# Kernel tuning notes

Hardware: AMD Instinct MI355X
Metric: run time of the kernel (lower is better)

Reference implementation:

```python
import jax, jax.numpy as jnp
import numpy as np

B, N, K, C = 8, 8192, 16, 64
POS_HID, MULT = 64, 4
BN_EPS = 1e-3  # keras BatchNormalization default


def _bn(x, gamma, beta):
    # inference-mode BN with init moving stats (mean=0, var=1)
    return gamma * x * (1.0 / np.sqrt(1.0 + BN_EPS)) + beta


def setup_inputs() -> dict:
    key = jax.random.key(0)
    ks = jax.random.split(key, 16)
    d = {
        "key": jax.random.normal(ks[0], (B, N, C), jnp.float32),
        "query": jax.random.normal(ks[1], (B, N, C), jnp.float32),
        "value": jax.random.normal(ks[2], (B, N, C), jnp.float32),
        "pos": jax.random.normal(ks[3], (B, N, 3), jnp.float32),
        "idx": jax.random.randint(ks[4], (B, N, K), 0, N, jnp.int32),
        # pos_conv1: 1x1 conv 3 -> POS_HID (glorot), + BN params
        "W1": jax.random.normal(ks[5], (3, POS_HID), jnp.float32) * np.sqrt(2.0 / (3 + POS_HID)),
        "b1": jnp.zeros((POS_HID,), jnp.float32),
        "g1": jnp.ones((POS_HID,), jnp.float32) + 0.1 * jax.random.normal(ks[6], (POS_HID,), jnp.float32),
        "bt1": 0.1 * jax.random.normal(ks[7], (POS_HID,), jnp.float32),
        # pos_conv2: POS_HID -> C, no activation
        "W2": jax.random.normal(ks[8], (POS_HID, C), jnp.float32) * np.sqrt(2.0 / (POS_HID + C)),
        "b2": jnp.zeros((C,), jnp.float32),
        # attn_mlp1: C -> MULT*C, BN + relu
        "W3": jax.random.normal(ks[9], (C, MULT * C), jnp.float32) * np.sqrt(2.0 / (C + MULT * C)),
        "b3": jnp.zeros((MULT * C,), jnp.float32),
        "g3": jnp.ones((MULT * C,), jnp.float32) + 0.1 * jax.random.normal(ks[10], (MULT * C,), jnp.float32),
        "bt3": 0.1 * jax.random.normal(ks[11], (MULT * C,), jnp.float32),
        # attn_mlp2: MULT*C -> C, no activation
        "W4": jax.random.normal(ks[12], (MULT * C, C), jnp.float32) * np.sqrt(2.0 / (MULT * C + C)),
        "b4": jnp.zeros((C,), jnp.float32),
    }
    return d


def reference(key, query, value, pos, idx, W1, b1, g1, bt1, W2, b2, W3, b3, g3, bt3, W4, b4):
    # per-batch KNN gather: key [B,N,C], idx [B,N,K] -> [B,N,K,C]
    gather = jax.vmap(lambda t, i: t[i])
    k_nb = gather(key, idx)                         # [B,N,K,C]
    qk_rel = query[:, :, None, :] - k_nb            # [B,N,K,C]
    pos_rel = pos[:, :, None, :] - gather(pos, idx)  # [B,N,K,3]

    # positional embedding MLP (1x1 convs)
    h = jax.nn.relu(_bn(pos_rel @ W1 + b1, g1, bt1))  # [B,N,K,POS_HID]
    pos_em = h @ W2 + b2                              # [B,N,K,C]

    # attention MLP (subtraction-based vector attention)
    a = jax.nn.relu(_bn((qk_rel + pos_em) @ W3 + b3, g3, bt3))  # [B,N,K,4C]
    a = (a @ W4 + b4) / jnp.sqrt(jnp.asarray(C, jnp.float32))   # [B,N,K,C]
    # tf.nn.softmax default axis=-1 -> softmax over CHANNEL axis (faithful to source)
    a = jax.nn.softmax(a, axis=-1)

    v = value[:, :, None, :] + pos_em               # [B,N,K,C]
    # einsum 'b c i j, b c i j -> b c j' on channels-last: sum over neighbor axis K
    agg = jnp.sum(a * v, axis=2)                    # [B,N,C]
    return agg
```

## Files before the change

### kernel.cpp

```cpp
#include <hip/hip_runtime.h>
#include <hip/hip_bf16.h>

typedef __bf16 bf16x8 __attribute__((ext_vector_type(8)));
typedef float  f32x4  __attribute__((ext_vector_type(4)));

#define MFMA16(A,B,C) __builtin_amdgcn_mfma_f32_16x16x32_bf16((A),(B),(C),0,0,0)

constexpr int NB = 8, NN = 8192, KK = 16;
constexpr size_t WS_NEEDED = 75776;


__global__ void prep_kernel(const float* __restrict__ W1, const float* __restrict__ b1,
                            const float* __restrict__ g1, const float* __restrict__ bt1,
                            const float* __restrict__ W2, const float* __restrict__ W3,
                            const float* __restrict__ b3, const float* __restrict__ g3,
                            const float* __restrict__ bt3, const float* __restrict__ W4,
                            unsigned char* __restrict__ ws)
{
    __bf16* w3f = (__bf16*)(ws);
    __bf16* w4f = (__bf16*)(ws + 32768);
    __bf16* w2f = (__bf16*)(ws + 65536);
    float*  W1f = (float*)(ws + 73728);
    float*  c1f = (float*)(ws + 74496);
    float*  c3f = (float*)(ws + 74752);

    const float inv = 1.0f / sqrtf(1.0f + 1e-3f);
    int t = blockIdx.x * 256 + threadIdx.x;

    if (t < 16384) {
        int i = t & 7, lane = (t >> 3) & 63, r = t >> 9;
        int ks = r & 1, nb = r >> 1;
        int k = ks * 32 + (lane >> 4) * 8 + i;
        int n = nb * 16 + (lane & 15);
        w3f[t] = (__bf16)(W3[k * 256 + n] * (g3[n] * inv));
    } else if (t < 32768) {
        int u = t - 16384;
        int i = u & 7, lane = (u >> 3) & 63, r = u >> 9;
        int kb = r & 7, nb = r >> 3;
        int k = kb * 32 + (lane >> 4) * 8 + i;
        int n = nb * 16 + (lane & 15);
        w4f[u] = (__bf16)(W4[k * 64 + n] * 0.125f);
    } else if (t < 36864) {
        int u = t - 32768;
        int i = u & 7, lane = (u >> 3) & 63, r = u >> 9;
        int ks = r & 1, nb = r >> 1;
        int k = ks * 32 + (lane >> 4) * 8 + i;
        int n = nb * 16 + (lane & 15);
        w2f[u] = (__bf16)(W2[k * 64 + n]);
    } else if (t < 37056) {
        int u = t - 36864;
        int c = u & 63;
        W1f[u] = W1[u] * (g1[c] * inv);
    } else if (t < 37120) {
        int c = t - 37056;
        c1f[c] = b1[c] * (g1[c] * inv) + bt1[c];
    } else if (t < 37376) {
        int n = t - 37120;
        c3f[n] = b3[n] * (g3[n] * inv) + bt3[n];
    }
}

__global__ __launch_bounds__(256, 2) void fused_kernel(
    const float* __restrict__ key, const float* __restrict__ query,
    const float* __restrict__ value, const float* __restrict__ pos,
    const int* __restrict__ idx, const float* __restrict__ b2,
    const float* __restrict__ b4, const unsigned char* __restrict__ ws,
    float* __restrict__ out)
{
    const __bf16* w3f = (const __bf16*)(ws);
    const __bf16* w4f = (const __bf16*)(ws + 32768);
    const __bf16* w2f = (const __bf16*)(ws + 65536);
    const float*  W1f = (const float*)(ws + 73728);
    const float*  c1f = (const float*)(ws + 74496);
    const float*  c3f = (const float*)(ws + 74752);

    __shared__ __attribute__((aligned(16))) __bf16 sX [4][2048];
    __shared__ __attribute__((aligned(16))) __bf16 sA1[4][2048];
    __shared__ __attribute__((aligned(16))) float  sPR[4][32][4];
    __shared__ int sJ[4][32];

    const int wv   = threadIdx.x >> 6;
    const int lane = threadIdx.x & 63;
    const int lg   = lane >> 4;
    const int ln   = lane & 15;

    const int ptbase = blockIdx.x * 8 + wv * 2;
    const int b  = ptbase >> 13;
    const int n0 = ptbase & 8191;

    __bf16* X  = sX[wv];
    __bf16* A1 = sA1[wv];

    if (lane < 32) {
        int p = lane >> 4, k = lane & 15;
        int n = n0 + p;
        int j = idx[(b * NN + n) * KK + k];
        sJ[wv][lane] = j;
        int pb = (b * NN + n) * 3, jb = (b * NN + j) * 3;
        sPR[wv][lane][0] = pos[pb + 0] - pos[jb + 0];
        sPR[wv][lane][1] = pos[pb + 1] - pos[jb + 1];
        sPR[wv][lane][2] = pos[pb + 2] - pos[jb + 2];
        sPR[wv][lane][3] = 0.f;
    }
    {
        float w0 = W1f[lane], w1 = W1f[64 + lane], w2c = W1f[128 + lane], cc1 = c1f[lane];
        for (int r = 0; r < 32; ++r) {
            float4 pr = *(const float4*)&sPR[wv][r][0];
            float hv = fmaf(pr.x, w0, fmaf(pr.y, w1, fmaf(pr.z, w2c, cc1)));
            hv = fmaxf(hv, 0.f);
            X[(r * 64 + lane) ^ ((r & 7) << 3)] = (__bf16)hv;
        }
    }

    bf16x8 hf[2][2];
    #pragma unroll
    for (int rb = 0; rb < 2; ++rb)
        #pragma unroll
        for (int ks = 0; ks < 2; ++ks) {
            int row = rb * 16 + ln;
            hf[rb][ks] = *(const bf16x8*)&X[(row * 64 + ks * 32 + lg * 8) ^ ((row & 7) << 3)];
        }
    f32x4 pacc[2][4];
    #pragma unroll
    for (int rb = 0; rb < 2; ++rb)
        #pragma unroll
        for (int cb = 0; cb < 4; ++cb) pacc[rb][cb] = f32x4{0.f, 0.f, 0.f, 0.f};
    #pragma unroll
    for (int cb = 0; cb < 4; ++cb)
        #pragma unroll
        for (int ks = 0; ks < 2; ++ks) {
            bf16x8 wf = *(const bf16x8*)(w2f + (size_t)((cb * 2 + ks) * 64 + lane) * 8);
            pacc[0][cb] = MFMA16(hf[0][ks], wf, pacc[0][cb]);
            pacc[1][cb] = MFMA16(hf[1][ks], wf, pacc[1][cb]);
        }

    float posem[2][4][4];
    #pragma unroll
    for (int rb = 0; rb < 2; ++rb) {
        const int nrow = n0 + rb;
        float qv[4];
        #pragma unroll
        for (int cb = 0; cb < 4; ++cb) {
            qv[cb] = query[(b * NN + nrow) * 64 + cb * 16 + ln];
            float c2v = b2[cb * 16 + ln];
            #pragma unroll
            for (int jj = 0; jj < 4; ++jj)
                posem[rb][cb][jj] = pacc[rb][cb][jj] + c2v;
        }
        #pragma unroll
        for (int jj = 0; jj < 4; ++jj) {
            int row = rb * 16 + lg * 4 + jj;
            int jb = (b * NN + sJ[wv][row]) * 64;
            #pragma unroll
            for (int cb = 0; cb < 4; ++cb) {
                float x = qv[cb] - key[jb + cb * 16 + ln] + posem[rb][cb][jj];
                X[(row * 64 + cb * 16 + ln) ^ ((row & 7) << 3)] = (__bf16)x;
            }
        }
    }

    bf16x8 xf[2][2];
    #pragma unroll
    for (int rb = 0; rb < 2; ++rb)
        #pragma unroll
        for (int ks = 0; ks < 2; ++ks) {
            int row = rb * 16 + ln;
            xf[rb][ks] = *(const bf16x8*)&X[(row * 64 + ks * 32 + lg * 8) ^ ((row & 7) << 3)];
        }
    f32x4 acc2[2][4];
    #pragma unroll
    for (int rb = 0; rb < 2; ++rb)
        #pragma unroll
        for (int nb = 0; nb < 4; ++nb) acc2[rb][nb] = f32x4{0.f, 0.f, 0.f, 0.f};

    for (int cc = 0; cc < 4; ++cc) {
        f32x4 g1a[2][4];
        #pragma unroll
        for (int rb = 0; rb < 2; ++rb)
            #pragma unroll
            for (int cb = 0; cb < 4; ++cb) g1a[rb][cb] = f32x4{0.f, 0.f, 0.f, 0.f};
        #pragma unroll
        for (int cb = 0; cb < 4; ++cb) {
            int nb = cc * 4 + cb;
            #pragma unroll
            for (int ks = 0; ks < 2; ++ks) {
                bf16x8 wf = *(const bf16x8*)(w3f + (size_t)((nb * 2 + ks) * 64 + lane) * 8);
                g1a[0][cb] = MFMA16(xf[0][ks], wf, g1a[0][cb]);
                g1a[1][cb] = MFMA16(xf[1][ks], wf, g1a[1][cb]);
            }
        }
        #pragma unroll
        for (int cb = 0; cb < 4; ++cb) {
            float c3v = c3f[(cc * 4 + cb) * 16 + ln];
            #pragma unroll
            for (int rb = 0; rb < 2; ++rb)
                #pragma unroll
                for (int jj = 0; jj < 4; ++jj) {
                    int row = rb * 16 + lg * 4 + jj;
                    float v = fmaxf(g1a[rb][cb][jj] + c3v, 0.f);
                    A1[(row * 64 + cb * 16 + ln) ^ ((row & 7) << 3)] = (__bf16)v;
                }
        }
        #pragma unroll
        for (int kb2 = 0; kb2 < 2; ++kb2) {
            bf16x8 a1f[2];
            #pragma unroll
            for (int rb = 0; rb < 2; ++rb) {
                int row = rb * 16 + ln;
                a1f[rb] = *(const bf16x8*)&A1[(row * 64 + kb2 * 32 + lg * 8) ^ ((row & 7) << 3)];
            }
            #pragma unroll
            for (int nb = 0; nb < 4; ++nb) {
                bf16x8 wf = *(const bf16x8*)(w4f + (size_t)((nb * 8 + cc * 2 + kb2) * 64 + lane) * 8);
                acc2[0][nb] = MFMA16(a1f[0], wf, acc2[0][nb]);
                acc2[1][nb] = MFMA16(a1f[1], wf, acc2[1][nb]);
            }
        }
    }

    #pragma unroll
    for (int rb = 0; rb < 2; ++rb) {
        const int nrow = n0 + rb;
        float val[4][4];
        #pragma unroll
        for (int nb = 0; nb < 4; ++nb) {
            float b4v = b4[nb * 16 + ln] * 0.125f;
            #pragma unroll
            for (int jj = 0; jj < 4; ++jj) val[nb][jj] = acc2[rb][nb][jj] + b4v;
        }
        float vv[4];
        #pragma unroll
        for (int nb = 0; nb < 4; ++nb) vv[nb] = value[(b * NN + nrow) * 64 + nb * 16 + ln];

        float res[4] = {0.f, 0.f, 0.f, 0.f};
        #pragma unroll
        for (int jj = 0; jj < 4; ++jj) {
            float m = fmaxf(fmaxf(val[0][jj], val[1][jj]), fmaxf(val[2][jj], val[3][jj]));
            #pragma unroll
            for (int d = 1; d < 16; d <<= 1) m = fmaxf(m, __shfl_xor(m, d, 64));
            float e0 = __expf(val[0][jj] - m), e1 = __expf(val[1][jj] - m);
            float e2 = __expf(val[2][jj] - m), e3 = __expf(val[3][jj] - m);
            float s = e0 + e1 + e2 + e3;
            #pragma unroll
            for (int d = 1; d < 16; d <<= 1) s += __shfl_xor(s, d, 64);
            float inv = 1.0f / s;
            res[0] = fmaf(e0 * inv, vv[0] + posem[rb][0][jj], res[0]);
            res[1] = fmaf(e1 * inv, vv[1] + posem[rb][1][jj], res[1]);
            res[2] = fmaf(e2 * inv, vv[2] + posem[rb][2][jj], res[2]);
            res[3] = fmaf(e3 * inv, vv[3] + posem[rb][3][jj], res[3]);
        }
        #pragma unroll
        for (int nb = 0; nb < 4; ++nb) {
            res[nb] += __shfl_xor(res[nb], 16, 64);
            res[nb] += __shfl_xor(res[nb], 32, 64);
        }
        float o = (lg == 0) ? res[0] : (lg == 1) ? res[1] : (lg == 2) ? res[2] : res[3];
        out[(b * NN + nrow) * 64 + lane] = o;
    }
}

extern "C" void kernel_launch(void* const* d_in, const int* in_sizes, int n_in,
                              void* d_out, int out_size, void* d_ws, size_t ws_size,
                              hipStream_t stream) {
    const float* key   = (const float*)d_in[0];
    const float* query = (const float*)d_in[1];
    const float* value = (const float*)d_in[2];
    const float* pos   = (const float*)d_in[3];
    const int*   idx   = (const int*)d_in[4];
    const float* W1    = (const float*)d_in[5];
    const float* b1    = (const float*)d_in[6];
    const float* g1    = (const float*)d_in[7];
    const float* bt1   = (const float*)d_in[8];
    const float* W2    = (const float*)d_in[9];
    const float* b2    = (const float*)d_in[10];
    const float* W3    = (const float*)d_in[11];
    const float* b3    = (const float*)d_in[12];
    const float* g3    = (const float*)d_in[13];
    const float* bt3   = (const float*)d_in[14];
    const float* W4    = (const float*)d_in[15];
    const float* b4    = (const float*)d_in[16];
    unsigned char* ws  = (unsigned char*)d_ws;
    float* out = (float*)d_out;

    if (ws_size < WS_NEEDED) return;

    hipLaunchKernelGGL(prep_kernel, dim3(146), dim3(256), 0, stream,
                       W1, b1, g1, bt1, W2, W3, b3, g3, bt3, W4, ws);
    hipLaunchKernelGGL(fused_kernel, dim3(8192), dim3(256), 0, stream,
                       key, query, value, pos, idx, b2, b4, ws, out);
}
```

Before: 305.1 us.

## Permute channel layout for vector LDS stores, MFMA pos-conv1, drop softmax max

Permutes the K dimension of W2/W3/W4 in the prep kernel so each lane can write its four channel values as one bf16x4 store into a padded (stride 72) LDS tile, replacing the XOR-swizzled scalar stores. The first positional 1x1 conv (3->64 with folded bias) now runs as an MFMA with a homogeneous-coordinate column instead of a scalar loop over 32 rows. The softmax max-subtraction and its shuffle reduction are removed, which risks overflow if logits grow large.

After: 262.0 us. -14.1%, faster.

```diff
diff --git a/kernel.cpp b/kernel.cpp
--- a/kernel.cpp
+++ b/kernel.cpp
@@ -2,12 +2,14 @@
 #include <hip/hip_bf16.h>
 
 typedef __bf16 bf16x8 __attribute__((ext_vector_type(8)));
+typedef __bf16 bf16x4 __attribute__((ext_vector_type(4)));
 typedef float  f32x4  __attribute__((ext_vector_type(4)));
 
 #define MFMA16(A,B,C) __builtin_amdgcn_mfma_f32_16x16x32_bf16((A),(B),(C),0,0,0)
 
 constexpr int NB = 8, NN = 8192, KK = 16;
-constexpr size_t WS_NEEDED = 75776;
+constexpr int XS = 72;
+constexpr size_t WS_NEEDED = 78848;
 
 
 __global__ void prep_kernel(const float* __restrict__ W1, const float* __restrict__ b1,
@@ -20,9 +22,8 @@
     __bf16* w3f = (__bf16*)(ws);
     __bf16* w4f = (__bf16*)(ws + 32768);
     __bf16* w2f = (__bf16*)(ws + 65536);
-    float*  W1f = (float*)(ws + 73728);
-    float*  c1f = (float*)(ws + 74496);
-    float*  c3f = (float*)(ws + 74752);
+    __bf16* w1f = (__bf16*)(ws + 73728);
+    float*  c3f = (float*)(ws + 77824);
 
     const float inv = 1.0f / sqrtf(1.0f + 1e-3f);
     int t = blockIdx.x * 256 + threadIdx.x;
@@ -30,32 +31,37 @@
     if (t < 16384) {
         int i = t & 7, lane = (t >> 3) & 63, r = t >> 9;
         int ks = r & 1, nb = r >> 1;
-        int k = ks * 32 + (lane >> 4) * 8 + i;
+        int p = ks * 32 + (lane >> 4) * 8 + i;
+        int c = (p & 3) * 16 + (p >> 2);
         int n = nb * 16 + (lane & 15);
-        w3f[t] = (__bf16)(W3[k * 256 + n] * (g3[n] * inv));
+        w3f[t] = (__bf16)(W3[c * 256 + n] * (g3[n] * inv));
     } else if (t < 32768) {
         int u = t - 16384;
         int i = u & 7, lane = (u >> 3) & 63, r = u >> 9;
         int kb = r & 7, nb = r >> 3;
-        int k = kb * 32 + (lane >> 4) * 8 + i;
+        int q = (kb & 1) * 32 + (lane >> 4) * 8 + i;
+        int c = (kb >> 1) * 64 + (q & 3) * 16 + (q >> 2);
         int n = nb * 16 + (lane & 15);
-        w4f[u] = (__bf16)(W4[k * 64 + n] * 0.125f);
+        w4f[u] = (__bf16)(W4[c * 64 + n] * 0.125f);
     } else if (t < 36864) {
         int u = t - 32768;
         int i = u & 7, lane = (u >> 3) & 63, r = u >> 9;
         int ks = r & 1, nb = r >> 1;
-        int k = ks * 32 + (lane >> 4) * 8 + i;
+        int p = ks * 32 + (lane >> 4) * 8 + i;
+        int c = (p & 3) * 16 + (p >> 2);
         int n = nb * 16 + (lane & 15);
-        w2f[u] = (__bf16)(W2[k * 64 + n]);
-    } else if (t < 37056) {
+        w2f[u] = (__bf16)(W2[c * 64 + n]);
+    } else if (t < 38912) {
         int u = t - 36864;
-        int c = u & 63;
-        W1f[u] = W1[u] * (g1[c] * inv);
-    } else if (t < 37120) {
-        int c = t - 37056;
-        c1f[c] = b1[c] * (g1[c] * inv) + bt1[c];
-    } else if (t < 37376) {
-        int n = t - 37120;
+        int i = u & 7, lane = (u >> 3) & 63, nb = u >> 9;
+        int kk = (lane >> 4) * 8 + i;
+        int n = nb * 16 + (lane & 15);
+        float v = 0.f;
+        if (kk < 3)       v = W1[kk * 64 + n] * (g1[n] * inv);
+        else if (kk == 3) v = b1[n] * (g1[n] * inv) + bt1[n];
+        w1f[u] = (__bf16)v;
+    } else if (t < 39168) {
+        int n = t - 38912;
         c3f[n] = b3[n] * (g3[n] * inv) + bt3[n];
     }
 }
@@ -70,12 +76,13 @@
     const __bf16* w3f = (const __bf16*)(ws);
     const __bf16* w4f = (const __bf16*)(ws + 32768);
     const __bf16* w2f = (const __bf16*)(ws + 65536);
-    const float*  W1f = (const float*)(ws + 73728);
-    const float*  c1f = (const float*)(ws + 74496);
-    const float*  c3f = (const float*)(ws + 74752);
-
-    __shared__ __attribute__((aligned(16))) __bf16 sX [4][2048];
-    __shared__ __attribute__((aligned(16))) __bf16 sA1[4][2048];
+    const __bf16* w1f = (const __bf16*)(ws + 73728);
+    const float*  c3f = (const float*)(ws + 77824);
+
+    const f32x4 ZERO4 = {0.f, 0.f, 0.f, 0.f};
+
+    __shared__ __attribute__((aligned(16))) __bf16 sX [4][32 * XS];
+    __shared__ __attribute__((aligned(16))) __bf16 sA1[4][32 * XS];
     __shared__ __attribute__((aligned(16))) float  sPR[4][32][4];
     __shared__ int sJ[4][32];
 
@@ -102,29 +109,48 @@
         sPR[wv][lane][2] = pos[pb + 2] - pos[jb + 2];
         sPR[wv][lane][3] = 0.f;
     }
-    {
-        float w0 = W1f[lane], w1 = W1f[64 + lane], w2c = W1f[128 + lane], cc1 = c1f[lane];
-        for (int r = 0; r < 32; ++r) {
-            float4 pr = *(const float4*)&sPR[wv][r][0];
-            float hv = fmaf(pr.x, w0, fmaf(pr.y, w1, fmaf(pr.z, w2c, cc1)));
-            hv = fmaxf(hv, 0.f);
-            X[(r * 64 + lane) ^ ((r & 7) << 3)] = (__bf16)hv;
-        }
-    }
+    bf16x8 af[2];
+    #pragma unroll
+    for (int rb = 0; rb < 2; ++rb) {
+        bf16x8 a;
+        #pragma unroll
+        for (int i = 0; i < 8; ++i) a[i] = (__bf16)0.0f;
+        if (lg == 0) {
+            const float4 pr = *(const float4*)&sPR[wv][rb * 16 + ln][0];
+            a[0] = (__bf16)pr.x; a[1] = (__bf16)pr.y; a[2] = (__bf16)pr.z;
+            a[3] = (__bf16)1.0f;
+        }
+        af[rb] = a;
+    }
+    f32x4 pa[2][4];
+    #pragma unroll
+    for (int nb = 0; nb < 4; ++nb) {
+        bf16x8 wf = *(const bf16x8*)(w1f + (size_t)(nb * 64 + lane) * 8);
+        pa[0][nb] = MFMA16(af[0], wf, ZERO4);
+        pa[1][nb] = MFMA16(af[1], wf, ZERO4);
+    }
+    #pragma unroll
+    for (int rb = 0; rb < 2; ++rb)
+        #pragma unroll
+        for (int jj = 0; jj < 4; ++jj) {
+            int row = rb * 16 + lg * 4 + jj;
+            bf16x4 hv;
+            #pragma unroll
+            for (int nb = 0; nb < 4; ++nb) hv[nb] = (__bf16)fmaxf(pa[rb][nb][jj], 0.f);
+            *(bf16x4*)&X[row * XS + ln * 4] = hv;
+        }
 
     bf16x8 hf[2][2];
     #pragma unroll
     for (int rb = 0; rb < 2; ++rb)
         #pragma unroll
-        for (int ks = 0; ks < 2; ++ks) {
-            int row = rb * 16 + ln;
-            hf[rb][ks] = *(const bf16x8*)&X[(row * 64 + ks * 32 + lg * 8) ^ ((row & 7) << 3)];
-        }
+        for (int ks = 0; ks < 2; ++ks)
+            hf[rb][ks] = *(const bf16x8*)&X[(rb * 16 + ln) * XS + ks * 32 + lg * 8];
     f32x4 pacc[2][4];
     #pragma unroll
     for (int rb = 0; rb < 2; ++rb)
         #pragma unroll
-        for (int cb = 0; cb < 4; ++cb) pacc[rb][cb] = f32x4{0.f, 0.f, 0.f, 0.f};
+        for (int cb = 0; cb < 4; ++cb) pacc[rb][cb] = ZERO4;
     #pragma unroll
     for (int cb = 0; cb < 4; ++cb)
         #pragma unroll
@@ -151,11 +177,11 @@
         for (int jj = 0; jj < 4; ++jj) {
             int row = rb * 16 + lg * 4 + jj;
             int jb = (b * NN + sJ[wv][row]) * 64;
-            #pragma unroll
-            for (int cb = 0; cb < 4; ++cb) {
-                float x = qv[cb] - key[jb + cb * 16 + ln] + posem[rb][cb][jj];
-                X[(row * 64 + cb * 16 + ln) ^ ((row & 7) << 3)] = (__bf16)x;
-            }
+            bf16x4 xv;
+            #pragma unroll
+            for (int cb = 0; cb < 4; ++cb)
+                xv[cb] = (__bf16)(qv[cb] - key[jb + cb * 16 + ln] + posem[rb][cb][jj]);
+            *(bf16x4*)&X[row * XS + ln * 4] = xv;
         }
     }
 
@@ -163,22 +189,20 @@
     #pragma unroll
     for (int rb = 0; rb < 2; ++rb)
         #pragma unroll
-        for (int ks = 0; ks < 2; ++ks) {
-            int row = rb * 16 + ln;
-            xf[rb][ks] = *(const bf16x8*)&X[(row * 64 + ks * 32 + lg * 8) ^ ((row & 7) << 3)];
-        }
+        for (int ks = 0; ks < 2; ++ks)
+            xf[rb][ks] = *(const bf16x8*)&X[(rb * 16 + ln) * XS + ks * 32 + lg * 8];
     f32x4 acc2[2][4];
     #pragma unroll
     for (int rb = 0; rb < 2; ++rb)
         #pragma unroll
-        for (int nb = 0; nb < 4; ++nb) acc2[rb][nb] = f32x4{0.f, 0.f, 0.f, 0.f};
+        for (int nb = 0; nb < 4; ++nb) acc2[rb][nb] = ZERO4;
 
     for (int cc = 0; cc < 4; ++cc) {
         f32x4 g1a[2][4];
         #pragma unroll
         for (int rb = 0; rb < 2; ++rb)
             #pragma unroll
-            for (int cb = 0; cb < 4; ++cb) g1a[rb][cb] = f32x4{0.f, 0.f, 0.f, 0.f};
+            for (int cb = 0; cb < 4; ++cb) g1a[rb][cb] = ZERO4;
         #pragma unroll
         for (int cb = 0; cb < 4; ++cb) {
             int nb = cc * 4 + cb;
@@ -189,26 +213,26 @@
                 g1a[1][cb] = MFMA16(xf[1][ks], wf, g1a[1][cb]);
             }
         }
-        #pragma unroll
-        for (int cb = 0; cb < 4; ++cb) {
-            float c3v = c3f[(cc * 4 + cb) * 16 + ln];
-            #pragma unroll
-            for (int rb = 0; rb < 2; ++rb)
+        float c3v[4];
+        #pragma unroll
+        for (int cb = 0; cb < 4; ++cb) c3v[cb] = c3f[(cc * 4 + cb) * 16 + ln];
+        #pragma unroll
+        for (int rb = 0; rb < 2; ++rb)
+            #pragma unroll
+            for (int jj = 0; jj < 4; ++jj) {
+                int row = rb * 16 + lg * 4 + jj;
+                bf16x4 av;
                 #pragma unroll
-                for (int jj = 0; jj < 4; ++jj) {
-                    int row = rb * 16 + lg * 4 + jj;
-                    float v = fmaxf(g1a[rb][cb][jj] + c3v, 0.f);
-                    A1[(row * 64 + cb * 16 + ln) ^ ((row & 7) << 3)] = (__bf16)v;
-                }
-        }
+                for (int cb = 0; cb < 4; ++cb)
+                    av[cb] = (__bf16)fmaxf(g1a[rb][cb][jj] + c3v[cb], 0.f);
+                *(bf16x4*)&A1[row * XS + ln * 4] = av;
+            }
         #pragma unroll
         for (int kb2 = 0; kb2 < 2; ++kb2) {
             bf16x8 a1f[2];
             #pragma unroll
-            for (int rb = 0; rb < 2; ++rb) {
-                int row = rb * 16 + ln;
-                a1f[rb] = *(const bf16x8*)&A1[(row * 64 + kb2 * 32 + lg * 8) ^ ((row & 7) << 3)];
-            }
+            for (int rb = 0; rb < 2; ++rb)
+                a1f[rb] = *(const bf16x8*)&A1[(rb * 16 + ln) * XS + kb2 * 32 + lg * 8];
             #pragma unroll
             for (int nb = 0; nb < 4; ++nb) {
                 bf16x8 wf = *(const bf16x8*)(w4f + (size_t)((nb * 8 + cc * 2 + kb2) * 64 + lane) * 8);
@@ -218,16 +242,12 @@
         }
     }
 
+    float b4v[4];
+    #pragma unroll
+    for (int nb = 0; nb < 4; ++nb) b4v[nb] = b4[nb * 16 + ln] * 0.125f;
     #pragma unroll
     for (int rb = 0; rb < 2; ++rb) {
         const int nrow = n0 + rb;
-        float val[4][4];
-        #pragma unroll
-        for (int nb = 0; nb < 4; ++nb) {
-            float b4v = b4[nb * 16 + ln] * 0.125f;
-            #pragma unroll
-            for (int jj = 0; jj < 4; ++jj) val[nb][jj] = acc2[rb][nb][jj] + b4v;
-        }
         float vv[4];
         #pragma unroll
         for (int nb = 0; nb < 4; ++nb) vv[nb] = value[(b * NN + nrow) * 64 + nb * 16 + ln];
@@ -235,12 +255,11 @@
         float res[4] = {0.f, 0.f, 0.f, 0.f};
         #pragma unroll
         for (int jj = 0; jj < 4; ++jj) {
-            float m = fmaxf(fmaxf(val[0][jj], val[1][jj]), fmaxf(val[2][jj], val[3][jj]));
-            #pragma unroll
-            for (int d = 1; d < 16; d <<= 1) m = fmaxf(m, __shfl_xor(m, d, 64));
-            float e0 = __expf(val[0][jj] - m), e1 = __expf(val[1][jj] - m);
-            float e2 = __expf(val[2][jj] - m), e3 = __expf(val[3][jj] - m);
-            float s = e0 + e1 + e2 + e3;
+            float e0 = __expf(acc2[rb][0][jj] + b4v[0]);
+            float e1 = __expf(acc2[rb][1][jj] + b4v[1]);
+            float e2 = __expf(acc2[rb][2][jj] + b4v[2]);
+            float e3 = __expf(acc2[rb][3][jj] + b4v[3]);
+            float s = (e0 + e1) + (e2 + e3);
             #pragma unroll
             for (int d = 1; d < 16; d <<= 1) s += __shfl_xor(s, d, 64);
             float inv = 1.0f / s;
@@ -284,7 +303,7 @@
 
     if (ws_size < WS_NEEDED) return;
 
-    hipLaunchKernelGGL(prep_kernel, dim3(146), dim3(256), 0, stream,
+    hipLaunchKernelGGL(prep_kernel, dim3(153), dim3(256), 0, stream,
                        W1, b1, g1, bt1, W2, W3, b3, g3, bt3, W4, ws);
     hipLaunchKernelGGL(fused_kernel, dim3(8192), dim3(256), 0, stream,
                        key, query, value, pos, idx, b2, b4, ws, out);
```
